# Kernel tuning notes

Measured on AMD Instinct MI355X. Metric: run time of the kernel, lower is better.

Reference implementation:

```python
import jax, jax.numpy as jnp
import numpy as np

N, IN_DIM, OUT_DIM, HEADS = 50000, 128, 32, 8
E = 800000
F = OUT_DIM * HEADS  # 256 fused output features
SEM_HID = 128        # SemanticAttention hidden size (HAN default)


def setup_inputs() -> dict:
    key = jax.random.key(0)
    ks = jax.random.split(key, 16)
    inp = {
        "h": jax.random.normal(ks[0], (N, IN_DIM), jnp.float32),
        "src_a": jax.random.randint(ks[1], (E,), 0, N, jnp.int32),
        "dst_a": jax.random.randint(ks[2], (E,), 0, N, jnp.int32),
        "src_b": jax.random.randint(ks[3], (E,), 0, N, jnp.int32),
        "dst_b": jax.random.randint(ks[4], (E,), 0, N, jnp.int32),
    }
    s = 1.0 / np.sqrt(IN_DIM)
    # per-metapath GATConv params
    inp["W_a"] = jax.random.normal(ks[5], (IN_DIM, F), jnp.float32) * s
    inp["al_a"] = jax.random.normal(ks[6], (HEADS, OUT_DIM), jnp.float32) * 0.1
    inp["ar_a"] = jax.random.normal(ks[7], (HEADS, OUT_DIM), jnp.float32) * 0.1
    inp["bias_a"] = jnp.zeros((F,), jnp.float32)
    inp["W_b"] = jax.random.normal(ks[8], (IN_DIM, F), jnp.float32) * s
    inp["al_b"] = jax.random.normal(ks[9], (HEADS, OUT_DIM), jnp.float32) * 0.1
    inp["ar_b"] = jax.random.normal(ks[10], (HEADS, OUT_DIM), jnp.float32) * 0.1
    inp["bias_b"] = jnp.zeros((F,), jnp.float32)
    # semantic attention params
    inp["Wsem"] = jax.random.normal(ks[11], (F, SEM_HID), jnp.float32) / np.sqrt(F)
    inp["bsem"] = jnp.zeros((SEM_HID,), jnp.float32)
    inp["wsem"] = jax.random.normal(ks[12], (SEM_HID,), jnp.float32) / np.sqrt(SEM_HID)
    return inp


def gat_conv(h, src, dst, W, al, ar, bias):
    # h: [N, in_dim] -> feat: [N, H, D]
    feat = (h @ W).reshape(N, HEADS, OUT_DIM)
    el = (feat * al).sum(-1)  # [N, H]
    er = (feat * ar).sum(-1)  # [N, H]
    e = jax.nn.leaky_relu(el[src] + er[dst], 0.2)  # [E, H]
    # edge softmax over incoming edges of each dst node (numerically stable)
    m = jax.ops.segment_max(e, dst, num_segments=N)        # -inf for empty
    ex = jnp.exp(e - m[dst])                               # [E, H]
    denom = jax.ops.segment_sum(ex, dst, num_segments=N)   # [N, H]
    msg = feat[src] * ex[:, :, None]                       # [E, H, D]
    out = jax.ops.segment_sum(msg, dst, num_segments=N)    # [N, H, D]
    out = out / jnp.where(denom > 0, denom, 1.0)[:, :, None]
    return jax.nn.elu(out.reshape(N, F) + bias)


def reference(h, src_a, dst_a, src_b, dst_b,
              W_a, al_a, ar_a, bias_a,
              W_b, al_b, ar_b, bias_b,
              Wsem, bsem, wsem):
    z_a = gat_conv(h, src_a, dst_a, W_a, al_a, ar_a, bias_a)
    z_b = gat_conv(h, src_b, dst_b, W_b, al_b, ar_b, bias_b)
    z = jnp.stack([z_a, z_b], axis=1)                 # [N, M, F]
    q = jnp.tanh(z @ Wsem + bsem) @ wsem              # [N, M]
    beta = jax.nn.softmax(q.mean(axis=0))             # [M]
    return (z * beta[None, :, None]).sum(axis=1)      # [N, F]
```

## Files before the change

### kernel.cpp

```cpp
#include <hip/hip_runtime.h>
#include <stdint.h>

#define NN 50000
#define EE 800000
#define IN_DIM 128
#define OUT_DIM 32
#define HEADS 8
#define FF 256
#define SH 128
#define NPAD 50048
#define FEXT 272
#define CAP 64
#define CSTRIDE 16

#define GEMM_BLKS 782
#define FILL_G   6250

#define P_BTA0   128
#define P_BTB0   (P_BTA0 + FEXT)
#define P_G      (P_BTB0 + FEXT)

#define F_GEMM   (2 * GEMM_BLKS)
#define F_G      (F_GEMM + FILL_G)

#define PULL_G   12500
#define C_G      (2 * PULL_G)
#define D_G      (2 * GEMM_BLKS)

typedef short s16x8 __attribute__((ext_vector_type(8)));
typedef float f32x4 __attribute__((ext_vector_type(4)));
typedef float f32x2 __attribute__((ext_vector_type(2)));

__device__ __forceinline__ float b2f(unsigned short u) {
    union { unsigned int i; float f; } v; v.i = ((unsigned int)u) << 16; return v.f;
}
__device__ __forceinline__ unsigned short f2b(float f) {
    union { float f; unsigned int i; } v; v.f = f;
    unsigned int i = v.i;
    unsigned int r = (i + 0x7FFFu + ((i >> 16) & 1u)) >> 16;
    return (unsigned short)r;
}

__device__ __forceinline__ void buildBT_one(
    const float* __restrict__ W, const float* __restrict__ al,
    const float* __restrict__ ar, unsigned short* __restrict__ BT,
    int fp, int k)
{
    float v;
    if (fp < FF) {
        v = W[(size_t)k * FF + fp];
    } else if (fp < FF + 8) {
        int hh = fp - FF;
        float s = 0.f;
        #pragma unroll
        for (int d = 0; d < 32; ++d) s += W[(size_t)k * FF + hh * 32 + d] * al[hh * 32 + d];
        v = s;
    } else {
        int hh = fp - FF - 8;
        float s = 0.f;
        #pragma unroll
        for (int d = 0; d < 32; ++d) s += W[(size_t)k * FF + hh * 32 + d] * ar[hh * 32 + d];
        v = s;
    }
    BT[(size_t)fp * IN_DIM + k] = f2b(v);
}

__global__ __launch_bounds__(256) void prep(
    const float* __restrict__ Wsem, unsigned short* __restrict__ WsemT,
    const float* __restrict__ W_a, const float* __restrict__ al_a,
    const float* __restrict__ ar_a, unsigned short* __restrict__ BT_a,
    const float* __restrict__ W_b, const float* __restrict__ al_b,
    const float* __restrict__ ar_b, unsigned short* __restrict__ BT_b)
{
    int b = blockIdx.x, t = threadIdx.x;
    if (b < P_BTA0) {
        WsemT[b * FF + t] = f2b(Wsem[(size_t)t * SH + b]);
    } else if (b < P_BTB0) {
        if (t < IN_DIM) buildBT_one(W_a, al_a, ar_a, BT_a, b - P_BTA0, t);
    } else {
        if (t < IN_DIM) buildBT_one(W_b, al_b, ar_b, BT_b, b - P_BTB0, t);
    }
}

__global__ __launch_bounds__(256) void megaF(
    const float* __restrict__ h,
    const unsigned short* __restrict__ BT_a, const unsigned short* __restrict__ BT_b,
    unsigned short* __restrict__ feat_a, unsigned short* __restrict__ feat_b,
    float* __restrict__ el_a, float* __restrict__ er_a,
    float* __restrict__ el_b, float* __restrict__ er_b,
    const int* __restrict__ src_a, const int* __restrict__ dst_a,
    const int* __restrict__ src_b, const int* __restrict__ dst_b,
    int* __restrict__ counts_a, int* __restrict__ counts_b,
    unsigned short* __restrict__ perm_a, unsigned short* __restrict__ perm_b)
{
    int b = blockIdx.x, t = threadIdx.x;
    if (b >= F_GEMM) {
        int idx = (b - F_GEMM) * 256 + t;
        if (idx < EE) {
            int d = dst_a[idx];
            int r = atomicAdd(&counts_a[d * CSTRIDE], 1);
            if (r < CAP) perm_a[d * CAP + r] = (unsigned short)src_a[idx];
        } else {
            int e = idx - EE;
            int d = dst_b[e];
            int r = atomicAdd(&counts_b[d * CSTRIDE], 1);
            if (r < CAP) perm_b[d * CAP + r] = (unsigned short)src_b[e];
        }
        return;
    }
    int mp = (b >= GEMM_BLKS);
    int gb = mp ? b - GEMM_BLKS : b;
    const unsigned short* BT = mp ? BT_b : BT_a;
    unsigned short* feat = mp ? feat_b : feat_a;
    float* el = mp ? el_b : el_a;
    float* er = mp ? er_b : er_a;

    int wave = t >> 6, lane = t & 63;
    int quad = lane >> 4, l16 = lane & 15;
    int nbase = gb * 64 + wave * 16;
    int n = nbase + l16;
    int nr = (n < NN) ? n : (NN - 1);
    const float* hrow = h + (size_t)nr * IN_DIM + quad * 8;
    s16x8 nfr[4];
    #pragma unroll
    for (int kt = 0; kt < 4; ++kt) {
        float4 p0 = *(const float4*)(hrow + kt * 32);
        float4 p1 = *(const float4*)(hrow + kt * 32 + 4);
        s16x8 v;
        v[0] = (short)f2b(p0.x); v[1] = (short)f2b(p0.y);
        v[2] = (short)f2b(p0.z); v[3] = (short)f2b(p0.w);
        v[4] = (short)f2b(p1.x); v[5] = (short)f2b(p1.y);
        v[6] = (short)f2b(p1.z); v[7] = (short)f2b(p1.w);
        nfr[kt] = v;
    }
    bool live = (n < NN);
    #pragma unroll 1
    for (int ft = 0; ft < 17; ++ft) {
        const unsigned short* brow = BT + (size_t)(ft * 16 + l16) * IN_DIM + quad * 8;
        f32x4 c = {0.f, 0.f, 0.f, 0.f};
        #pragma unroll
        for (int kt = 0; kt < 4; ++kt) {
            s16x8 ffr = *(const s16x8*)(brow + kt * 32);
            c = __builtin_amdgcn_mfma_f32_16x16x32_bf16(ffr, nfr[kt], c, 0, 0, 0);
        }
        if (ft < 16) {
            if (live) {
                ushort4 r;
                r.x = f2b(c[0]); r.y = f2b(c[1]); r.z = f2b(c[2]); r.w = f2b(c[3]);
                *(ushort4*)(feat + (size_t)n * FF + ft * 16 + quad * 4) = r;
            }
        } else if (live) {
            #pragma unroll
            for (int r = 0; r < 4; ++r) {
                int jp = quad * 4 + r;
                if (jp < 8) el[n * HEADS + jp] = c[r];
                else        er[n * HEADS + (jp - 8)] = c[r];
            }
        }
    }
}

__global__ __launch_bounds__(256, 8) void megaC(
    const int* __restrict__ counts_a, const int* __restrict__ counts_b,
    const unsigned short* __restrict__ perm_a, const unsigned short* __restrict__ perm_b,
    const float* __restrict__ el_a, const float* __restrict__ er_a,
    const float* __restrict__ el_b, const float* __restrict__ er_b,
    const unsigned short* __restrict__ feat_a, const unsigned short* __restrict__ feat_b,
    const float* __restrict__ bias_a, const float* __restrict__ bias_b,
    unsigned short* __restrict__ zb_a, unsigned short* __restrict__ zb_b)
{
    int bb = blockIdx.x;
    int mp = (bb >= PULL_G);
    int blk = mp ? bb - PULL_G : bb;
    const int* counts = mp ? counts_b : counts_a;
    const unsigned short* perm = mp ? perm_b : perm_a;
    const float* el = mp ? el_b : el_a;
    const float* er = mp ? er_b : er_a;
    const unsigned short* feat = mp ? feat_b : feat_a;
    const float* bias = mp ? bias_b : bias_a;
    unsigned short* zb = mp ? zb_b : zb_a;

    int wave = threadIdx.x >> 6;
    int lane = threadIdx.x & 63;
    int n = blk * 4 + wave;
    int sub = lane >> 5;
    int l32 = lane & 31;
    int head = l32 >> 2;
    int fbase = l32 * 8;
    int deg = counts[n * CSTRIDE];
    if (deg > CAP) deg = CAP;
    int base = n * CAP;
    float ern = er[n * HEADS + head];
    float den = 0.f;
    f32x2 acc2[4];
    #pragma unroll
    for (int u = 0; u < 4; ++u) { acc2[u][0] = 0.f; acc2[u][1] = 0.f; }

#define PROC(EV, FV) {                                               \
        float x = (EV) + ern;                                        \
        x = fmaxf(x, 0.2f * x);                                      \
        float ex = __expf(x);                                        \
        den += ex;                                                   \
        f32x2 ex2; ex2[0] = ex; ex2[1] = ex;                         \
        const unsigned int* fp = (const unsigned int*)&(FV);         \
        _Pragma("unroll")                                            \
        for (int u = 0; u < 4; ++u) {                                \
            union { unsigned int i; float f; } lo, hi;               \
            lo.i = fp[u] << 16; hi.i = fp[u] & 0xFFFF0000u;          \
            f32x2 v; v[0] = lo.f; v[1] = hi.f;                       \
            acc2[u] += v * ex2;                                      \
        } }

    int jp = sub;
    #pragma unroll 1
    for (; jp + 6 < deg; jp += 8) {
        int s0 = perm[base + jp];
        int s1 = perm[base + jp + 2];
        int s2 = perm[base + jp + 4];
        int s3 = perm[base + jp + 6];
        float e0 = el[s0 * HEADS + head];
        float e1 = el[s1 * HEADS + head];
        float e2 = el[s2 * HEADS + head];
        float e3 = el[s3 * HEADS + head];
        uint4 f0 = *(const uint4*)(feat + (size_t)s0 * FF + fbase);
        uint4 f1 = *(const uint4*)(feat + (size_t)s1 * FF + fbase);
        uint4 f2 = *(const uint4*)(feat + (size_t)s2 * FF + fbase);
        uint4 f3 = *(const uint4*)(feat + (size_t)s3 * FF + fbase);
        PROC(e0, f0); PROC(e1, f1); PROC(e2, f2); PROC(e3, f3);
    }
    #pragma unroll 1
    for (; jp + 2 < deg; jp += 4) {
        int s0 = perm[base + jp];
        int s1 = perm[base + jp + 2];
        float e0 = el[s0 * HEADS + head];
        float e1 = el[s1 * HEADS + head];
        uint4 f0 = *(const uint4*)(feat + (size_t)s0 * FF + fbase);
        uint4 f1 = *(const uint4*)(feat + (size_t)s1 * FF + fbase);
        PROC(e0, f0); PROC(e1, f1);
    }
    if (jp < deg) {
        int s0 = perm[base + jp];
        float e0 = el[s0 * HEADS + head];
        uint4 f0 = *(const uint4*)(feat + (size_t)s0 * FF + fbase);
        PROC(e0, f0);
    }
#undef PROC

    float accf[8];
    #pragma unroll
    for (int u = 0; u < 4; ++u) {
        accf[2 * u]     = acc2[u][0];
        accf[2 * u + 1] = acc2[u][1];
    }

    den += __shfl_xor(den, 32, 64);
    #pragma unroll
    for (int u = 0; u < 8; ++u) accf[u] += __shfl_xor(accf[u], 32, 64);

    if (den <= 0.f) den = 1.f;
    float inv = 1.f / den;
    float4 b0 = *(const float4*)(bias + fbase);
    float4 b1 = *(const float4*)(bias + fbase + 4);
    float bv[8] = {b0.x, b0.y, b0.z, b0.w, b1.x, b1.y, b1.z, b1.w};
    if (sub == 0) {
        ushort4 r0, r1;
        unsigned short rr[8];
        #pragma unroll
        for (int u = 0; u < 8; ++u) {
            float ov = accf[u] * inv + bv[u];
            ov = (ov > 0.f) ? ov : (__expf(ov) - 1.f);
            rr[u] = f2b(ov);
        }
        r0.x = rr[0]; r0.y = rr[1]; r0.z = rr[2]; r0.w = rr[3];
        r1.x = rr[4]; r1.y = rr[5]; r1.z = rr[6]; r1.w = rr[7];
        *(ushort4*)(zb + (size_t)n * FF + fbase) = r0;
        *(ushort4*)(zb + (size_t)n * FF + fbase + 4) = r1;
    }
}

__global__ __launch_bounds__(256) void megaD(
    const unsigned short* __restrict__ zb_a, const unsigned short* __restrict__ zb_b,
    const unsigned short* __restrict__ WsemT,
    const float* __restrict__ bsem, const float* __restrict__ wsem,
    float* __restrict__ qsum)
{
    int bb = blockIdx.x;
    int mp = (bb >= GEMM_BLKS);
    int blk = mp ? bb - GEMM_BLKS : bb;
    const unsigned short* zb = mp ? zb_b : zb_a;

    int wave = threadIdx.x >> 6, lane = threadIdx.x & 63;
    int quad = lane >> 4, l16 = lane & 15;
    int nbase = blk * 64 + wave * 16;
    const unsigned short* arow = zb + (size_t)(nbase + l16) * FF + quad * 8;
    s16x8 afr[8];
    #pragma unroll
    for (int kt = 0; kt < 8; ++kt)
        afr[kt] = *(const s16x8*)(arow + kt * 32);
    float qacc = 0.f;
    for (int jt = 0; jt < 8; ++jt) {
        int jj = jt * 16 + l16;
        const unsigned short* brow = WsemT + (size_t)jj * FF + quad * 8;
        f32x4 c = {0.f, 0.f, 0.f, 0.f};
        #pragma unroll
        for (int kt = 0; kt < 8; ++kt) {
            s16x8 bfr = *(const s16x8*)(brow + kt * 32);
            c = __builtin_amdgcn_mfma_f32_16x16x32_bf16(afr[kt], bfr, c, 0, 0, 0);
        }
        float bj = bsem[jj], wj = wsem[jj];
        #pragma unroll
        for (int r = 0; r < 4; ++r) {
            int n = nbase + quad * 4 + r;
            float y = c[r] + bj;
            y = fminf(fmaxf(y, -10.f), 10.f);
            float t = __expf(2.f * y);
            float tv = (t - 1.f) * __builtin_amdgcn_rcpf(t + 1.f) * wj;
            qacc += (n < NN) ? tv : 0.f;
        }
    }
    #pragma unroll
    for (int o = 1; o < 64; o <<= 1) qacc += __shfl_xor(qacc, o, 64);
    __shared__ float wsum[4];
    if (lane == 0) wsum[wave] = qacc;
    __syncthreads();
    if (threadIdx.x == 0)
        atomicAdd(&qsum[mp], wsum[0] + wsum[1] + wsum[2] + wsum[3]);
}

__global__ __launch_bounds__(256) void combine_kernel(
    const unsigned short* __restrict__ za,
    const unsigned short* __restrict__ zbm,
    float* __restrict__ out, const float* __restrict__ qsum)
{
    size_t i = (size_t)blockIdx.x * blockDim.x + threadIdx.x;
    size_t base = i * 4;
    if (base >= (size_t)NN * FF) return;
    float qa = qsum[0] * (1.f / NN), qb = qsum[1] * (1.f / NN);
    float mx = fmaxf(qa, qb);
    float ea = __expf(qa - mx), eb = __expf(qb - mx);
    float inv = 1.f / (ea + eb);
    float b0 = ea * inv, b1 = eb * inv;
    ushort4 va = *(const ushort4*)(za + base);
    ushort4 vb = *(const ushort4*)(zbm + base);
    float4 r;
    r.x = b0 * b2f(va.x) + b1 * b2f(vb.x);
    r.y = b0 * b2f(va.y) + b1 * b2f(vb.y);
    r.z = b0 * b2f(va.z) + b1 * b2f(vb.z);
    r.w = b0 * b2f(va.w) + b1 * b2f(vb.w);
    *(float4*)(out + base) = r;
}

extern "C" void kernel_launch(void* const* d_in, const int* in_sizes, int n_in,
                              void* d_out, int out_size, void* d_ws, size_t ws_size,
                              hipStream_t stream)
{
    const float* h      = (const float*)d_in[0];
    const int* src_a    = (const int*)d_in[1];
    const int* dst_a    = (const int*)d_in[2];
    const int* src_b    = (const int*)d_in[3];
    const int* dst_b    = (const int*)d_in[4];
    const float* W_a    = (const float*)d_in[5];
    const float* al_a   = (const float*)d_in[6];
    const float* ar_a   = (const float*)d_in[7];
    const float* bias_a = (const float*)d_in[8];
    const float* W_b    = (const float*)d_in[9];
    const float* al_b   = (const float*)d_in[10];
    const float* ar_b   = (const float*)d_in[11];
    const float* bias_b = (const float*)d_in[12];
    const float* Wsem   = (const float*)d_in[13];
    const float* bsem   = (const float*)d_in[14];
    const float* wsem   = (const float*)d_in[15];
    float* out = (float*)d_out;

    char* ws = (char*)d_ws;
    size_t o = 0;
    auto alloc = [&](size_t bytes) -> char* {
        char* p = ws + o;
        o += (bytes + 255) & ~(size_t)255;
        return p;
    };
    unsigned short* BT_a   = (unsigned short*)alloc((size_t)FEXT * IN_DIM * 2);
    unsigned short* BT_b   = (unsigned short*)alloc((size_t)FEXT * IN_DIM * 2);
    unsigned short* feat_a = (unsigned short*)alloc((size_t)NN * FF * 2);
    unsigned short* feat_b = (unsigned short*)alloc((size_t)NN * FF * 2);
    unsigned short* zb_a   = (unsigned short*)alloc((size_t)NPAD * FF * 2);
    unsigned short* zb_b   = (unsigned short*)alloc((size_t)NPAD * FF * 2);
    unsigned short* WsemT  = (unsigned short*)alloc((size_t)SH * FF * 2);
    float* el_a    = (float*)alloc((size_t)NN * HEADS * 4);
    float* er_a    = (float*)alloc((size_t)NN * HEADS * 4);
    float* el_b    = (float*)alloc((size_t)NN * HEADS * 4);
    float* er_b    = (float*)alloc((size_t)NN * HEADS * 4);
    unsigned short* perm_a = (unsigned short*)alloc((size_t)NN * CAP * 2);
    unsigned short* perm_b = (unsigned short*)alloc((size_t)NN * CAP * 2);
    char* zspan0   = ws + o;
    int* counts_a  = (int*)alloc((size_t)NN * CSTRIDE * 4);
    int* counts_b  = (int*)alloc((size_t)NN * CSTRIDE * 4);
    float* qsum    = (float*)alloc(8);
    size_t zspan   = (size_t)((ws + o) - zspan0);

    hipMemsetAsync(zspan0, 0, zspan, stream);
    prep<<<P_G, 256, 0, stream>>>(Wsem, WsemT,
                                  W_a, al_a, ar_a, BT_a,
                                  W_b, al_b, ar_b, BT_b);
    megaF<<<F_G, 256, 0, stream>>>(h, BT_a, BT_b, feat_a, feat_b,
                                   el_a, er_a, el_b, er_b,
                                   src_a, dst_a, src_b, dst_b,
                                   counts_a, counts_b, perm_a, perm_b);
    megaC<<<C_G, 256, 0, stream>>>(counts_a, counts_b, perm_a, perm_b,
                                   el_a, er_a, el_b, er_b,
                                   feat_a, feat_b, bias_a, bias_b, zb_a, zb_b);
    megaD<<<D_G, 256, 0, stream>>>(zb_a, zb_b, WsemT, bsem, wsem, qsum);
    combine_kernel<<<(int)(((size_t)NN * FF / 4 + 255) / 256), 256, 0, stream>>>(zb_a, zb_b, out, qsum);
}
```

Baseline: 458.6 us.

## Fuse semantic-attention GEMM into edge-aggregation kernel via shared-memory tile

Merges the semantic attention projection (megaD) into the aggregation kernel (megaC). Each block grows to 1024 threads covering 16 nodes and stages the bf16 outputs in LDS, then four waves run the MFMA projection with tanh and wsem reduction and atomically add into qsum. This removes one launch and the re-read of z from global memory. In exchange it adds a block barrier, more atomics (one per wave instead of one per block), and launch_bounds(1024,8) may squeeze registers and occupancy.

```diff
diff --git a/kernel.cpp b/kernel.cpp
--- a/kernel.cpp
+++ b/kernel.cpp
@@ -23,9 +23,9 @@
 #define F_GEMM   (2 * GEMM_BLKS)
 #define F_G      (F_GEMM + FILL_G)
 
-#define PULL_G   12500
-#define C_G      (2 * PULL_G)
-#define D_G      (2 * GEMM_BLKS)
+#define C_BLK    3125
+#define C_G      (2 * C_BLK)
+#define ZLD      264
 
 typedef short s16x8 __attribute__((ext_vector_type(8)));
 typedef float f32x4 __attribute__((ext_vector_type(4)));
@@ -160,18 +160,22 @@
     }
 }
 
-__global__ __launch_bounds__(256, 8) void megaC(
+__global__ __launch_bounds__(1024, 8) void megaC(
     const int* __restrict__ counts_a, const int* __restrict__ counts_b,
     const unsigned short* __restrict__ perm_a, const unsigned short* __restrict__ perm_b,
     const float* __restrict__ el_a, const float* __restrict__ er_a,
     const float* __restrict__ el_b, const float* __restrict__ er_b,
     const unsigned short* __restrict__ feat_a, const unsigned short* __restrict__ feat_b,
     const float* __restrict__ bias_a, const float* __restrict__ bias_b,
-    unsigned short* __restrict__ zb_a, unsigned short* __restrict__ zb_b)
-{
+    unsigned short* __restrict__ zb_a, unsigned short* __restrict__ zb_b,
+    const unsigned short* __restrict__ WsemT,
+    const float* __restrict__ bsem, const float* __restrict__ wsem,
+    float* __restrict__ qsum)
+{
+    __shared__ unsigned short zs[16][ZLD];
     int bb = blockIdx.x;
-    int mp = (bb >= PULL_G);
-    int blk = mp ? bb - PULL_G : bb;
+    int mp = (bb >= C_BLK);
+    int blk = mp ? bb - C_BLK : bb;
     const int* counts = mp ? counts_b : counts_a;
     const unsigned short* perm = mp ? perm_b : perm_a;
     const float* el = mp ? el_b : el_a;
@@ -182,7 +186,7 @@
 
     int wave = threadIdx.x >> 6;
     int lane = threadIdx.x & 63;
-    int n = blk * 4 + wave;
+    int n = blk * 16 + wave;
     int sub = lane >> 5;
     int l32 = lane & 31;
     int head = l32 >> 2;
@@ -275,56 +279,44 @@
         r1.x = rr[4]; r1.y = rr[5]; r1.z = rr[6]; r1.w = rr[7];
         *(ushort4*)(zb + (size_t)n * FF + fbase) = r0;
         *(ushort4*)(zb + (size_t)n * FF + fbase + 4) = r1;
-    }
-}
-
-__global__ __launch_bounds__(256) void megaD(
-    const unsigned short* __restrict__ zb_a, const unsigned short* __restrict__ zb_b,
-    const unsigned short* __restrict__ WsemT,
-    const float* __restrict__ bsem, const float* __restrict__ wsem,
-    float* __restrict__ qsum)
-{
-    int bb = blockIdx.x;
-    int mp = (bb >= GEMM_BLKS);
-    int blk = mp ? bb - GEMM_BLKS : bb;
-    const unsigned short* zb = mp ? zb_b : zb_a;
-
-    int wave = threadIdx.x >> 6, lane = threadIdx.x & 63;
-    int quad = lane >> 4, l16 = lane & 15;
-    int nbase = blk * 64 + wave * 16;
-    const unsigned short* arow = zb + (size_t)(nbase + l16) * FF + quad * 8;
-    s16x8 afr[8];
-    #pragma unroll
-    for (int kt = 0; kt < 8; ++kt)
-        afr[kt] = *(const s16x8*)(arow + kt * 32);
-    float qacc = 0.f;
-    for (int jt = 0; jt < 8; ++jt) {
-        int jj = jt * 16 + l16;
-        const unsigned short* brow = WsemT + (size_t)jj * FF + quad * 8;
-        f32x4 c = {0.f, 0.f, 0.f, 0.f};
-        #pragma unroll
-        for (int kt = 0; kt < 8; ++kt) {
-            s16x8 bfr = *(const s16x8*)(brow + kt * 32);
-            c = __builtin_amdgcn_mfma_f32_16x16x32_bf16(afr[kt], bfr, c, 0, 0, 0);
+        *(ushort4*)&zs[wave][fbase] = r0;
+        *(ushort4*)&zs[wave][fbase + 4] = r1;
+    }
+    __syncthreads();
+
+    if (wave < 4) {
+        int quad = lane >> 4, l16 = lane & 15;
+        int nbase = blk * 16;
+        s16x8 afr[8];
+        #pragma unroll
+        for (int kt = 0; kt < 8; ++kt)
+            afr[kt] = *(const s16x8*)&zs[l16][quad * 8 + kt * 32];
+        float qacc = 0.f;
+        #pragma unroll
+        for (int i = 0; i < 2; ++i) {
+            int jt = wave * 2 + i;
+            int jj = jt * 16 + l16;
+            const unsigned short* brow = WsemT + (size_t)jj * FF + quad * 8;
+            f32x4 c = {0.f, 0.f, 0.f, 0.f};
+            #pragma unroll
+            for (int kt = 0; kt < 8; ++kt) {
+                s16x8 bfr = *(const s16x8*)(brow + kt * 32);
+                c = __builtin_amdgcn_mfma_f32_16x16x32_bf16(afr[kt], bfr, c, 0, 0, 0);
+            }
+            float bj = bsem[jj], wj = wsem[jj];
+            #pragma unroll
+            for (int r = 0; r < 4; ++r) {
+                float y = c[r] + bj;
+                y = fminf(fmaxf(y, -10.f), 10.f);
+                float t = __expf(2.f * y);
+                qacc += (t - 1.f) * __builtin_amdgcn_rcpf(t + 1.f) * wj;
+            }
         }
-        float bj = bsem[jj], wj = wsem[jj];
-        #pragma unroll
-        for (int r = 0; r < 4; ++r) {
-            int n = nbase + quad * 4 + r;
-            float y = c[r] + bj;
-            y = fminf(fmaxf(y, -10.f), 10.f);
-            float t = __expf(2.f * y);
-            float tv = (t - 1.f) * __builtin_amdgcn_rcpf(t + 1.f) * wj;
-            qacc += (n < NN) ? tv : 0.f;
-        }
-    }
-    #pragma unroll
-    for (int o = 1; o < 64; o <<= 1) qacc += __shfl_xor(qacc, o, 64);
-    __shared__ float wsum[4];
-    if (lane == 0) wsum[wave] = qacc;
-    __syncthreads();
-    if (threadIdx.x == 0)
-        atomicAdd(&qsum[mp], wsum[0] + wsum[1] + wsum[2] + wsum[3]);
+        (void)nbase;
+        #pragma unroll
+        for (int o = 1; o < 64; o <<= 1) qacc += __shfl_xor(qacc, o, 64);
+        if (lane == 0) atomicAdd(&qsum[mp], qacc);
+    }
 }
 
 __global__ __launch_bounds__(256) void combine_kernel(
@@ -406,9 +398,9 @@
                                    el_a, er_a, el_b, er_b,
                                    src_a, dst_a, src_b, dst_b,
                                    counts_a, counts_b, perm_a, perm_b);
-    megaC<<<C_G, 256, 0, stream>>>(counts_a, counts_b, perm_a, perm_b,
-                                   el_a, er_a, el_b, er_b,
-                                   feat_a, feat_b, bias_a, bias_b, zb_a, zb_b);
-    megaD<<<D_G, 256, 0, stream>>>(zb_a, zb_b, WsemT, bsem, wsem, qsum);
+    megaC<<<C_G, 1024, 0, stream>>>(counts_a, counts_b, perm_a, perm_b,
+                                    el_a, er_a, el_b, er_b,
+                                    feat_a, feat_b, bias_a, bias_b, zb_a, zb_b,
+                                    WsemT, bsem, wsem, qsum);
     combine_kernel<<<(int)(((size_t)NN * FF / 4 + 255) / 256), 256, 0, stream>>>(zb_a, zb_b, out, qsum);
 }
```

Result: slower. 602.8 us (+31.4%).

## Software-pipeline the two metapaths across staggered fused kernels

Applied to the files above, without the earlier changes.

Reorganizes the four kernels into five stages that stagger metapath A and B work. Fill for A runs with weight prep, GEMM A with fill B, GEMM B with pull A, semantic A with pull B, then semantic B alone. The aim is to overlap compute-bound GEMM/MFMA blocks with memory and atomic-bound fill/pull blocks inside each launch, so each kernel mixes different resource demands. In exchange there is one more kernel launch and a serial tail stage for the last semantic pass.

```diff
diff --git a/kernel.cpp b/kernel.cpp
--- a/kernel.cpp
+++ b/kernel.cpp
@@ -14,18 +14,12 @@
 #define CSTRIDE 16
 
 #define GEMM_BLKS 782
-#define FILL_G   6250
+#define FILLH_G  3125
+#define PULLH_G  12500
 
 #define P_BTA0   128
 #define P_BTB0   (P_BTA0 + FEXT)
 #define P_G      (P_BTB0 + FEXT)
-
-#define F_GEMM   (2 * GEMM_BLKS)
-#define F_G      (F_GEMM + FILL_G)
-
-#define PULL_G   12500
-#define C_G      (2 * PULL_G)
-#define D_G      (2 * GEMM_BLKS)
 
 typedef short s16x8 __attribute__((ext_vector_type(8)));
 typedef float f32x4 __attribute__((ext_vector_type(4)));
@@ -65,56 +59,21 @@
     BT[(size_t)fp * IN_DIM + k] = f2b(v);
 }
 
-__global__ __launch_bounds__(256) void prep(
-    const float* __restrict__ Wsem, unsigned short* __restrict__ WsemT,
-    const float* __restrict__ W_a, const float* __restrict__ al_a,
-    const float* __restrict__ ar_a, unsigned short* __restrict__ BT_a,
-    const float* __restrict__ W_b, const float* __restrict__ al_b,
-    const float* __restrict__ ar_b, unsigned short* __restrict__ BT_b)
-{
-    int b = blockIdx.x, t = threadIdx.x;
-    if (b < P_BTA0) {
-        WsemT[b * FF + t] = f2b(Wsem[(size_t)t * SH + b]);
-    } else if (b < P_BTB0) {
-        if (t < IN_DIM) buildBT_one(W_a, al_a, ar_a, BT_a, b - P_BTA0, t);
-    } else {
-        if (t < IN_DIM) buildBT_one(W_b, al_b, ar_b, BT_b, b - P_BTB0, t);
-    }
-}
-
-__global__ __launch_bounds__(256) void megaF(
-    const float* __restrict__ h,
-    const unsigned short* __restrict__ BT_a, const unsigned short* __restrict__ BT_b,
-    unsigned short* __restrict__ feat_a, unsigned short* __restrict__ feat_b,
-    float* __restrict__ el_a, float* __restrict__ er_a,
-    float* __restrict__ el_b, float* __restrict__ er_b,
-    const int* __restrict__ src_a, const int* __restrict__ dst_a,
-    const int* __restrict__ src_b, const int* __restrict__ dst_b,
-    int* __restrict__ counts_a, int* __restrict__ counts_b,
-    unsigned short* __restrict__ perm_a, unsigned short* __restrict__ perm_b)
-{
-    int b = blockIdx.x, t = threadIdx.x;
-    if (b >= F_GEMM) {
-        int idx = (b - F_GEMM) * 256 + t;
-        if (idx < EE) {
-            int d = dst_a[idx];
-            int r = atomicAdd(&counts_a[d * CSTRIDE], 1);
-            if (r < CAP) perm_a[d * CAP + r] = (unsigned short)src_a[idx];
-        } else {
-            int e = idx - EE;
-            int d = dst_b[e];
-            int r = atomicAdd(&counts_b[d * CSTRIDE], 1);
-            if (r < CAP) perm_b[d * CAP + r] = (unsigned short)src_b[e];
-        }
-        return;
-    }
-    int mp = (b >= GEMM_BLKS);
-    int gb = mp ? b - GEMM_BLKS : b;
-    const unsigned short* BT = mp ? BT_b : BT_a;
-    unsigned short* feat = mp ? feat_b : feat_a;
-    float* el = mp ? el_b : el_a;
-    float* er = mp ? er_b : er_a;
-
+__device__ __forceinline__ void dev_fill(
+    int idx, const int* __restrict__ src, const int* __restrict__ dst,
+    int* __restrict__ counts, unsigned short* __restrict__ perm)
+{
+    int d = dst[idx];
+    int r = atomicAdd(&counts[d * CSTRIDE], 1);
+    if (r < CAP) perm[d * CAP + r] = (unsigned short)src[idx];
+}
+
+__device__ __forceinline__ void dev_gemm(
+    int gb, int t, const float* __restrict__ h,
+    const unsigned short* __restrict__ BT,
+    unsigned short* __restrict__ feat,
+    float* __restrict__ el, float* __restrict__ er)
+{
     int wave = t >> 6, lane = t & 63;
     int quad = lane >> 4, l16 = lane & 15;
     int nbase = gb * 64 + wave * 16;
@@ -160,28 +119,15 @@
     }
 }
 
-__global__ __launch_bounds__(256, 8) void megaC(
-    const int* __restrict__ counts_a, const int* __restrict__ counts_b,
-    const unsigned short* __restrict__ perm_a, const unsigned short* __restrict__ perm_b,
-    const float* __restrict__ el_a, const float* __restrict__ er_a,
-    const float* __restrict__ el_b, const float* __restrict__ er_b,
-    const unsigned short* __restrict__ feat_a, const unsigned short* __restrict__ feat_b,
-    const float* __restrict__ bias_a, const float* __restrict__ bias_b,
-    unsigned short* __restrict__ zb_a, unsigned short* __restrict__ zb_b)
-{
-    int bb = blockIdx.x;
-    int mp = (bb >= PULL_G);
-    int blk = mp ? bb - PULL_G : bb;
-    const int* counts = mp ? counts_b : counts_a;
-    const unsigned short* perm = mp ? perm_b : perm_a;
-    const float* el = mp ? el_b : el_a;
-    const float* er = mp ? er_b : er_a;
-    const unsigned short* feat = mp ? feat_b : feat_a;
-    const float* bias = mp ? bias_b : bias_a;
-    unsigned short* zb = mp ? zb_b : zb_a;
-
-    int wave = threadIdx.x >> 6;
-    int lane = threadIdx.x & 63;
+__device__ __forceinline__ void dev_pull(
+    int blk, int tid,
+    const int* __restrict__ counts, const unsigned short* __restrict__ perm,
+    const float* __restrict__ el, const float* __restrict__ er,
+    const unsigned short* __restrict__ feat, const float* __restrict__ bias,
+    unsigned short* __restrict__ zb)
+{
+    int wave = tid >> 6;
+    int lane = tid & 63;
     int n = blk * 4 + wave;
     int sub = lane >> 5;
     int l32 = lane & 31;
@@ -278,17 +224,13 @@
     }
 }
 
-__global__ __launch_bounds__(256) void megaD(
-    const unsigned short* __restrict__ zb_a, const unsigned short* __restrict__ zb_b,
+__device__ __forceinline__ void dev_semD(
+    int blk, const unsigned short* __restrict__ zb,
     const unsigned short* __restrict__ WsemT,
     const float* __restrict__ bsem, const float* __restrict__ wsem,
-    float* __restrict__ qsum)
-{
-    int bb = blockIdx.x;
-    int mp = (bb >= GEMM_BLKS);
-    int blk = mp ? bb - GEMM_BLKS : bb;
-    const unsigned short* zb = mp ? zb_b : zb_a;
-
+    float* __restrict__ qs)
+{
+    __shared__ float wsum[4];
     int wave = threadIdx.x >> 6, lane = threadIdx.x & 63;
     int quad = lane >> 4, l16 = lane & 15;
     int nbase = blk * 64 + wave * 16;
@@ -320,11 +262,93 @@
     }
     #pragma unroll
     for (int o = 1; o < 64; o <<= 1) qacc += __shfl_xor(qacc, o, 64);
-    __shared__ float wsum[4];
     if (lane == 0) wsum[wave] = qacc;
     __syncthreads();
     if (threadIdx.x == 0)
-        atomicAdd(&qsum[mp], wsum[0] + wsum[1] + wsum[2] + wsum[3]);
+        atomicAdd(qs, wsum[0] + wsum[1] + wsum[2] + wsum[3]);
+}
+
+
+__global__ __launch_bounds__(256) void stage1(
+    const float* __restrict__ Wsem, unsigned short* __restrict__ WsemT,
+    const float* __restrict__ W_a, const float* __restrict__ al_a,
+    const float* __restrict__ ar_a, unsigned short* __restrict__ BT_a,
+    const float* __restrict__ W_b, const float* __restrict__ al_b,
+    const float* __restrict__ ar_b, unsigned short* __restrict__ BT_b,
+    const int* __restrict__ src_a, const int* __restrict__ dst_a,
+    int* __restrict__ counts_a, unsigned short* __restrict__ perm_a)
+{
+    int b = blockIdx.x, t = threadIdx.x;
+    if (b < P_BTA0) {
+        WsemT[b * FF + t] = f2b(Wsem[(size_t)t * SH + b]);
+    } else if (b < P_BTB0) {
+        if (t < IN_DIM) buildBT_one(W_a, al_a, ar_a, BT_a, b - P_BTA0, t);
+    } else if (b < P_G) {
+        if (t < IN_DIM) buildBT_one(W_b, al_b, ar_b, BT_b, b - P_BTB0, t);
+    } else {
+        dev_fill((b - P_G) * 256 + t, src_a, dst_a, counts_a, perm_a);
+    }
+}
+
+__global__ __launch_bounds__(256) void stage2(
+    const float* __restrict__ h, const unsigned short* __restrict__ BT_a,
+    unsigned short* __restrict__ feat_a,
+    float* __restrict__ el_a, float* __restrict__ er_a,
+    const int* __restrict__ src_b, const int* __restrict__ dst_b,
+    int* __restrict__ counts_b, unsigned short* __restrict__ perm_b)
+{
+    int b = blockIdx.x, t = threadIdx.x;
+    if (b < GEMM_BLKS) {
+        dev_gemm(b, t, h, BT_a, feat_a, el_a, er_a);
+    } else {
+        dev_fill((b - GEMM_BLKS) * 256 + t, src_b, dst_b, counts_b, perm_b);
+    }
+}
+
+__global__ __launch_bounds__(256, 8) void stage3(
+    const float* __restrict__ h, const unsigned short* __restrict__ BT_b,
+    unsigned short* __restrict__ feat_b,
+    float* __restrict__ el_b, float* __restrict__ er_b,
+    const int* __restrict__ counts_a, const unsigned short* __restrict__ perm_a,
+    const float* __restrict__ el_a, const float* __restrict__ er_a,
+    const unsigned short* __restrict__ feat_a, const float* __restrict__ bias_a,
+    unsigned short* __restrict__ zb_a)
+{
+    int b = blockIdx.x;
+    if (b < GEMM_BLKS) {
+        dev_gemm(b, threadIdx.x, h, BT_b, feat_b, el_b, er_b);
+    } else {
+        dev_pull(b - GEMM_BLKS, threadIdx.x, counts_a, perm_a,
+                 el_a, er_a, feat_a, bias_a, zb_a);
+    }
+}
+
+__global__ __launch_bounds__(256, 8) void stage4(
+    const unsigned short* __restrict__ zb_a,
+    const unsigned short* __restrict__ WsemT,
+    const float* __restrict__ bsem, const float* __restrict__ wsem,
+    float* __restrict__ qsum,
+    const int* __restrict__ counts_b, const unsigned short* __restrict__ perm_b,
+    const float* __restrict__ el_b, const float* __restrict__ er_b,
+    const unsigned short* __restrict__ feat_b, const float* __restrict__ bias_b,
+    unsigned short* __restrict__ zb_b)
+{
+    int b = blockIdx.x;
+    if (b < GEMM_BLKS) {
+        dev_semD(b, zb_a, WsemT, bsem, wsem, &qsum[0]);
+    } else {
+        dev_pull(b - GEMM_BLKS, threadIdx.x, counts_b, perm_b,
+                 el_b, er_b, feat_b, bias_b, zb_b);
+    }
+}
+
+__global__ __launch_bounds__(256) void stage5(
+    const unsigned short* __restrict__ zb_b,
+    const unsigned short* __restrict__ WsemT,
+    const float* __restrict__ bsem, const float* __restrict__ wsem,
+    float* __restrict__ qsum)
+{
+    dev_semD(blockIdx.x, zb_b, WsemT, bsem, wsem, &qsum[1]);
 }
 
 __global__ __launch_bounds__(256) void combine_kernel(
@@ -399,16 +423,18 @@
     size_t zspan   = (size_t)((ws + o) - zspan0);
 
     hipMemsetAsync(zspan0, 0, zspan, stream);
-    prep<<<P_G, 256, 0, stream>>>(Wsem, WsemT,
-                                  W_a, al_a, ar_a, BT_a,
-                                  W_b, al_b, ar_b, BT_b);
-    megaF<<<F_G, 256, 0, stream>>>(h, BT_a, BT_b, feat_a, feat_b,
-                                   el_a, er_a, el_b, er_b,
-                                   src_a, dst_a, src_b, dst_b,
-                                   counts_a, counts_b, perm_a, perm_b);
-    megaC<<<C_G, 256, 0, stream>>>(counts_a, counts_b, perm_a, perm_b,
-                                   el_a, er_a, el_b, er_b,
-                                   feat_a, feat_b, bias_a, bias_b, zb_a, zb_b);
-    megaD<<<D_G, 256, 0, stream>>>(zb_a, zb_b, WsemT, bsem, wsem, qsum);
+    stage1<<<P_G + FILLH_G, 256, 0, stream>>>(
+        Wsem, WsemT, W_a, al_a, ar_a, BT_a, W_b, al_b, ar_b, BT_b,
+        src_a, dst_a, counts_a, perm_a);
+    stage2<<<GEMM_BLKS + FILLH_G, 256, 0, stream>>>(
+        h, BT_a, feat_a, el_a, er_a,
+        src_b, dst_b, counts_b, perm_b);
+    stage3<<<GEMM_BLKS + PULLH_G, 256, 0, stream>>>(
+        h, BT_b, feat_b, el_b, er_b,
+        counts_a, perm_a, el_a, er_a, feat_a, bias_a, zb_a);
+    stage4<<<GEMM_BLKS + PULLH_G, 256, 0, stream>>>(
+        zb_a, WsemT, bsem, wsem, qsum,
+        counts_b, perm_b, el_b, er_b, feat_b, bias_b, zb_b);
+    stage5<<<GEMM_BLKS, 256, 0, stream>>>(zb_b, WsemT, bsem, wsem, qsum);
     combine_kernel<<<(int)(((size_t)NN * FF / 4 + 255) / 256), 256, 0, stream>>>(zb_a, zb_b, out, qsum);
 }
```

After: 434.5 us. 1.06x faster.
